# Optimization experiments

Measured on AMD Instinct MI355X. Metric: run time of the kernel, lower is better.

The kernel has to match this reference:

```python
import jax, jax.numpy as jnp
import numpy as np

N_NODES = 50000
N_FEAT = 128
HIDDEN = 3
N_EDGES = 600000
N_POWERS = 3


def setup_inputs() -> dict:
    key = jax.random.key(0)
    ks = jax.random.split(key, 6)
    x = jax.random.normal(ks[0], (N_NODES, N_FEAT), dtype=jnp.float32)
    edge_index = jax.random.randint(ks[1], (N_POWERS, 2, N_EDGES), 0, N_NODES, dtype=jnp.int64)
    # MLP params for the 3 adjacency powers, stacked on the leading axis.
    # torch Linear(in,out) stored transposed here: y = x @ W + b.
    Wa = jax.random.normal(ks[2], (N_POWERS, N_FEAT, HIDDEN), dtype=jnp.float32) * (1.0 / np.sqrt(N_FEAT))
    ba = jax.random.normal(ks[3], (N_POWERS, HIDDEN), dtype=jnp.float32) * 0.01
    Wb = jax.random.normal(ks[4], (N_POWERS, HIDDEN, 1), dtype=jnp.float32) * (1.0 / np.sqrt(HIDDEN))
    bb = jax.random.normal(ks[5], (N_POWERS, 1), dtype=jnp.float32) * 0.01
    return {"x": x, "edge_index": edge_index, "Wa": Wa, "ba": ba, "Wb": Wb, "bb": bb}


def reference(x, edge_index, Wa, ba, Wb, bb):
    # Gather source/target node features per edge, per adjacency power.
    x_j = x[edge_index[:, 0]]          # [P, E, F]
    x_i = x[edge_index[:, 1]]          # [P, E, F]
    abs_dif = jnp.abs(x_j - x_i)       # [P, E, F]
    # Tiny per-edge MLP: Linear -> ReLU -> Linear -> Sigmoid (separate params per power).
    h = jax.nn.relu(jnp.einsum('pef,pfh->peh', abs_dif, Wa) + ba[:, None, :])  # [P, E, H]
    w = jax.nn.sigmoid(jnp.einsum('peh,pho->peo', h, Wb) + bb[:, None, :])     # [P, E, 1]
    return w[..., 0]                   # [P, E] edge weights for each power
```

## Files before the change

### kernel.cpp

```cpp
#include <hip/hip_runtime.h>
#include <math.h>

#define N_NODES 50000
#define N_FEAT  128
#define N_EDGES 600000
#define N_POWERS 3

#define PAIRS 5
#define EDGES_PER_BLK (64 * PAIRS)

#define CAP 81920
#define NBUCK 8
#define CHUNK 2048
#define NCHUNK 293

typedef _Float16 half2v __attribute__((ext_vector_type(2)));
union HU { unsigned u; half2v h; };

__device__ __forceinline__ int bucket_of(int j) { return (int)(((unsigned)j * 41u) >> 18); }

__global__ __launch_bounds__(256) void conv_x_plain(const float* __restrict__ x,
                                                    unsigned* __restrict__ xh,
                                                    const float* __restrict__ Wa,
                                                    unsigned* __restrict__ wah) {
    const int t = blockIdx.x * 256 + threadIdx.x;
    const float4* x4 = (const float4*)x;
    float4 a = x4[(size_t)t * 2];
    float4 b = x4[(size_t)t * 2 + 1];
    HU p0, p1, p2, p3;
    p0.h = half2v{(_Float16)a.x, (_Float16)a.y};
    p1.h = half2v{(_Float16)a.z, (_Float16)a.w};
    p2.h = half2v{(_Float16)b.x, (_Float16)b.y};
    p3.h = half2v{(_Float16)b.z, (_Float16)b.w};
    ((uint4*)xh)[t] = uint4{p0.u, p1.u, p2.u, p3.u};
    if (blockIdx.x == 0 && threadIdx.x < 192) {
        const int tt = threadIdx.x;
        #pragma unroll
        for (int q = 0; q < 3; ++q) {
            int idx = tt + q * 192;
            int c  = idx % 3;
            int pk = idx / 3;
            int k  = pk % 64;
            int p  = pk / 64;
            float w0 = Wa[p * 384 + (2 * k) * 3 + c];
            float w1 = Wa[p * 384 + (2 * k + 1) * 3 + c];
            HU u; u.h = half2v{(_Float16)w0, (_Float16)w1};
            wah[idx] = u.u;
        }
    }
}

__global__ __launch_bounds__(256) void hist_kernel(const int* __restrict__ edge_index,
                                                   int* __restrict__ hist) {
    __shared__ int lh[NBUCK];
    const int p = blockIdx.y, chunk = blockIdx.x;
    if (threadIdx.x < NBUCK) lh[threadIdx.x] = 0;
    __syncthreads();
    const int* ej = edge_index + (size_t)p * 2 * N_EDGES;
    const int base = chunk * CHUNK;
    #pragma unroll
    for (int k = 0; k < 8; ++k) {
        const int e = base + k * 256 + threadIdx.x;
        if (e < N_EDGES) {
            const int j = __builtin_nontemporal_load(ej + e);
            atomicAdd(&lh[bucket_of(j)], 1);
        }
    }
    __syncthreads();
    if (threadIdx.x < NBUCK)
        hist[(p * NBUCK + threadIdx.x) * NCHUNK + chunk] = lh[threadIdx.x];
}

__global__ __launch_bounds__(64) void scan_hist(int* __restrict__ hist,
                                                int* __restrict__ cur) {
    const int pb = blockIdx.x;
    const int lane = threadIdx.x;
    int* h = hist + pb * NCHUNK;
    int carry = 0;
    for (int t = 0; t < NCHUNK; t += 64) {
        const int c = t + lane;
        int v = (c < NCHUNK) ? h[c] : 0;
        int s = v;
        #pragma unroll
        for (int d = 1; d < 64; d <<= 1) {
            int u = __shfl_up(s, d, 64);
            if (lane >= d) s += u;
        }
        if (c < NCHUNK) h[c] = carry + (s - v);
        carry += __shfl(s, 63, 64);
    }
    if (lane == 0) cur[pb] = carry;
}

__global__ __launch_bounds__(256) void scatter_pass(const int* __restrict__ edge_index,
                                                    const int* __restrict__ hist,
                                                    unsigned long long* __restrict__ su) {
    __shared__ int lc[NBUCK];
    const int p = blockIdx.y, chunk = blockIdx.x;
    if (threadIdx.x < NBUCK) lc[threadIdx.x] = 0;
    __syncthreads();
    const int* ej = edge_index + (size_t)p * 2 * N_EDGES;
    const int* ei = ej + N_EDGES;
    const int base = chunk * CHUNK;
    #pragma unroll
    for (int k = 0; k < 8; ++k) {
        const int e = base + k * 256 + threadIdx.x;
        if (e < N_EDGES) {
            const int j = __builtin_nontemporal_load(ej + e);
            const int i = __builtin_nontemporal_load(ei + e);
            const int b = bucket_of(j);
            const int pos = atomicAdd(&lc[b], 1);
            const int off = hist[(p * NBUCK + b) * NCHUNK + chunk];
            const size_t slot = (size_t)(p * NBUCK + b) * CAP + off + pos;
            su[slot] = (unsigned long long)(unsigned)(j | (i << 16))
                     | ((unsigned long long)e << 32);
        }
    }
}

template<int PAT>
__device__ __forceinline__ float swz(float v) {
    return __int_as_float(__builtin_amdgcn_ds_swizzle(__float_as_int(v), PAT));
}

__device__ __forceinline__ void dot3_8(const uint4& qa0, const uint4& qa1,
                                       const uint4& qb0, const uint4& qb1,
                                       const HU wa[8][3],
                                       float& h0, float& h1, float& h2) {
    unsigned ua[8] = {qa0.x, qa0.y, qa0.z, qa0.w, qa1.x, qa1.y, qa1.z, qa1.w};
    unsigned ub[8] = {qb0.x, qb0.y, qb0.z, qb0.w, qb1.x, qb1.y, qb1.z, qb1.w};
    h0 = 0.f; h1 = 0.f; h2 = 0.f;
    #pragma unroll
    for (int k = 0; k < 8; ++k) {
        HU a, b, d;
        a.u = ua[k]; b.u = ub[k];
        d.h = a.h - b.h;
        d.u &= 0x7fff7fffu;
        h0 = __builtin_amdgcn_fdot2(d.h, wa[k][0].h, h0, false);
        h1 = __builtin_amdgcn_fdot2(d.h, wa[k][1].h, h1, false);
        h2 = __builtin_amdgcn_fdot2(d.h, wa[k][2].h, h2, false);
    }
}

__global__ __launch_bounds__(256) void adj_kernel_sorted(
    const unsigned* __restrict__ xh,
    const unsigned long long* __restrict__ su,
    const int* __restrict__ cur,
    const unsigned* __restrict__ wah,
    const float* __restrict__ ba,
    const float* __restrict__ Wb,
    const float* __restrict__ bb,
    float* __restrict__ out)
{
    const int p    = blockIdx.y;
    const int b    = blockIdx.x & 7;
    const int k    = blockIdx.x >> 3;
    const int tid  = threadIdx.x;
    const int lane = tid & 63;
    const int wave = tid >> 6;
    const int sub  = lane & 7;
    const int grp  = lane >> 3;

    const int count = cur[p * NBUCK + b];
    const int base  = k * EDGES_PER_BLK;
    if (base >= count) return;

    HU wa[8][3];
    {
        const unsigned* wp = wah + ((size_t)p * 64 + sub * 8) * 3;
        #pragma unroll
        for (int kk = 0; kk < 8; ++kk) {
            wa[kk][0].u = wp[kk * 3 + 0];
            wa[kk][1].u = wp[kk * 3 + 1];
            wa[kk][2].u = wp[kk * 3 + 2];
        }
        #pragma unroll
        for (int kk = 0; kk < 8; ++kk) {
            asm volatile("" : "+v"(wa[kk][0].u), "+v"(wa[kk][1].u), "+v"(wa[kk][2].u));
        }
    }

    const float ba0 = ba[p * 3 + 0], ba1 = ba[p * 3 + 1], ba2 = ba[p * 3 + 2];
    const float wb0 = Wb[p * 3 + 0], wb1 = Wb[p * 3 + 1], wb2 = Wb[p * 3 + 2];
    const float bbp = bb[p];

    const unsigned long long* sup = su + (size_t)(p * NBUCK + b) * CAP;
    float* outp = out + (size_t)p * N_EDGES;

    const int eoff = wave * 8 + grp;
    const int roff = sub * 8;
    const int cm1  = count - 1;

    #pragma unroll
    for (int it = 0; it < PAIRS; ++it) {
        const int r1 = base + it * 64 + eoff;
        const int r2 = r1 + 32;
        const bool v1 = r1 < count;
        const bool v2 = r2 < count;
        const int s1 = min(r1, cm1);
        const int s2 = min(r2, cm1);

        const unsigned long long q1 = __builtin_nontemporal_load(sup + s1);
        const unsigned long long q2 = __builtin_nontemporal_load(sup + s2);
        const int j1 = (int)(q1 & 0xFFFFu);
        const int i1 = (int)((q1 >> 16) & 0xFFFFu);
        const int e1 = (int)(q1 >> 32);
        const int j2 = (int)(q2 & 0xFFFFu);
        const int i2 = (int)((q2 >> 16) & 0xFFFFu);
        const int e2 = (int)(q2 >> 32);

        const uint4* rj1 = (const uint4*)(xh + ((size_t)j1 << 6) + roff);
        const uint4* ri1 = (const uint4*)(xh + ((size_t)i1 << 6) + roff);
        const uint4* rj2 = (const uint4*)(xh + ((size_t)j2 << 6) + roff);
        const uint4* ri2 = (const uint4*)(xh + ((size_t)i2 << 6) + roff);
        uint4 a0 = rj1[0], a1 = rj1[1];
        uint4 b0 = ri1[0], b1 = ri1[1];
        uint4 c0 = rj2[0], c1 = rj2[1];
        uint4 d0 = ri2[0], d1 = ri2[1];

        float h0a, h1a, h2a, h0b, h1b, h2b;
        dot3_8(a0, a1, b0, b1, wa, h0a, h1a, h2a);
        dot3_8(c0, c1, d0, d1, wa, h0b, h1b, h2b);

        h0a += swz<0x041F>(h0a); h1a += swz<0x041F>(h1a); h2a += swz<0x041F>(h2a);
        h0b += swz<0x041F>(h0b); h1b += swz<0x041F>(h1b); h2b += swz<0x041F>(h2b);
        h0a += swz<0x081F>(h0a); h1a += swz<0x081F>(h1a); h2a += swz<0x081F>(h2a);
        h0b += swz<0x081F>(h0b); h1b += swz<0x081F>(h1b); h2b += swz<0x081F>(h2b);
        h0a += swz<0x101F>(h0a); h1a += swz<0x101F>(h1a); h2a += swz<0x101F>(h2a);
        h0b += swz<0x101F>(h0b); h1b += swz<0x101F>(h1b); h2b += swz<0x101F>(h2b);

        if (sub == 0) {
            if (v1) {
                float r0 = fmaxf(h0a + ba0, 0.f);
                float r1f = fmaxf(h1a + ba1, 0.f);
                float r2f = fmaxf(h2a + ba2, 0.f);
                float s  = fmaf(r0, wb0, fmaf(r1f, wb1, fmaf(r2f, wb2, bbp)));
                __builtin_nontemporal_store(1.f / (1.f + __expf(-s)), outp + e1);
            }
            if (v2) {
                float r0 = fmaxf(h0b + ba0, 0.f);
                float r1f = fmaxf(h1b + ba1, 0.f);
                float r2f = fmaxf(h2b + ba2, 0.f);
                float s  = fmaf(r0, wb0, fmaf(r1f, wb1, fmaf(r2f, wb2, bbp)));
                __builtin_nontemporal_store(1.f / (1.f + __expf(-s)), outp + e2);
            }
        }
    }
}

__global__ __launch_bounds__(256) void adj_kernel_f16(
    const unsigned* __restrict__ xh,
    const unsigned* __restrict__ wah,
    const int*   __restrict__ edge_index,
    const float* __restrict__ ba,
    const float* __restrict__ Wb,
    const float* __restrict__ bb,
    float* __restrict__ out)
{
    const int p    = blockIdx.y;
    const int tid  = threadIdx.x;
    const int lane = tid & 63;
    const int wave = tid >> 6;
    const int sub  = lane & 7;
    const int grp  = lane >> 3;

    HU wa[8][3];
    {
        const unsigned* wp = wah + ((size_t)p * 64 + sub * 8) * 3;
        #pragma unroll
        for (int k = 0; k < 8; ++k) {
            wa[k][0].u = wp[k * 3 + 0];
            wa[k][1].u = wp[k * 3 + 1];
            wa[k][2].u = wp[k * 3 + 2];
        }
        #pragma unroll
        for (int k = 0; k < 8; ++k) {
            asm volatile("" : "+v"(wa[k][0].u), "+v"(wa[k][1].u), "+v"(wa[k][2].u));
        }
    }

    const float ba0 = ba[p * 3 + 0], ba1 = ba[p * 3 + 1], ba2 = ba[p * 3 + 2];
    const float wb0 = Wb[p * 3 + 0], wb1 = Wb[p * 3 + 1], wb2 = Wb[p * 3 + 2];
    const float bbp = bb[p];

    const int* ej = edge_index + (size_t)p * 2 * N_EDGES;
    const int* ei = ej + N_EDGES;
    float* outp = out + (size_t)p * N_EDGES;

    const int e_blk = blockIdx.x * EDGES_PER_BLK;
    const int eoff  = wave * 8 + grp;
    const int roff  = sub * 8;

    #pragma unroll
    for (int it = 0; it < PAIRS; ++it) {
        const int e1 = e_blk + it * 64 + eoff;
        const int e2 = e1 + 32;
        const int j1 = __builtin_nontemporal_load(ej + e1);
        const int i1 = __builtin_nontemporal_load(ei + e1);
        const int j2 = __builtin_nontemporal_load(ej + e2);
        const int i2 = __builtin_nontemporal_load(ei + e2);

        const uint4* rj1 = (const uint4*)(xh + ((size_t)j1 << 6) + roff);
        const uint4* ri1 = (const uint4*)(xh + ((size_t)i1 << 6) + roff);
        const uint4* rj2 = (const uint4*)(xh + ((size_t)j2 << 6) + roff);
        const uint4* ri2 = (const uint4*)(xh + ((size_t)i2 << 6) + roff);
        uint4 a0 = rj1[0], a1 = rj1[1];
        uint4 b0 = ri1[0], b1 = ri1[1];
        uint4 c0 = rj2[0], c1 = rj2[1];
        uint4 d0 = ri2[0], d1 = ri2[1];

        float h0a, h1a, h2a, h0b, h1b, h2b;
        dot3_8(a0, a1, b0, b1, wa, h0a, h1a, h2a);
        dot3_8(c0, c1, d0, d1, wa, h0b, h1b, h2b);

        h0a += swz<0x041F>(h0a); h1a += swz<0x041F>(h1a); h2a += swz<0x041F>(h2a);
        h0b += swz<0x041F>(h0b); h1b += swz<0x041F>(h1b); h2b += swz<0x041F>(h2b);
        h0a += swz<0x081F>(h0a); h1a += swz<0x081F>(h1a); h2a += swz<0x081F>(h2a);
        h0b += swz<0x081F>(h0b); h1b += swz<0x081F>(h1b); h2b += swz<0x081F>(h2b);
        h0a += swz<0x101F>(h0a); h1a += swz<0x101F>(h1a); h2a += swz<0x101F>(h2a);
        h0b += swz<0x101F>(h0b); h1b += swz<0x101F>(h1b); h2b += swz<0x101F>(h2b);

        if (sub == 0) {
            float r0 = fmaxf(h0a + ba0, 0.f);
            float r1 = fmaxf(h1a + ba1, 0.f);
            float r2 = fmaxf(h2a + ba2, 0.f);
            float s  = fmaf(r0, wb0, fmaf(r1, wb1, fmaf(r2, wb2, bbp)));
            __builtin_nontemporal_store(1.f / (1.f + __expf(-s)), outp + e1);
            r0 = fmaxf(h0b + ba0, 0.f);
            r1 = fmaxf(h1b + ba1, 0.f);
            r2 = fmaxf(h2b + ba2, 0.f);
            s  = fmaf(r0, wb0, fmaf(r1, wb1, fmaf(r2, wb2, bbp)));
            __builtin_nontemporal_store(1.f / (1.f + __expf(-s)), outp + e2);
        }
    }
}

__global__ __launch_bounds__(256) void adj_kernel_f32(
    const float* __restrict__ x,
    const int*   __restrict__ edge_index,
    const float* __restrict__ Wa,
    const float* __restrict__ ba,
    const float* __restrict__ Wb,
    const float* __restrict__ bb,
    float* __restrict__ out)
{
    const int p    = blockIdx.y;
    const int tid  = threadIdx.x;
    const int lane = tid & 63;
    const int wave = tid >> 6;
    const int sub  = lane & 15;
    const int grp  = lane >> 4;
    const int f0 = sub * 8;

    const float* Wap = Wa + (size_t)p * N_FEAT * 3;
    float wa0[8], wa1[8], wa2[8];
    #pragma unroll
    for (int k = 0; k < 8; ++k) {
        wa0[k] = Wap[(f0 + k) * 3 + 0];
        wa1[k] = Wap[(f0 + k) * 3 + 1];
        wa2[k] = Wap[(f0 + k) * 3 + 2];
    }
    const float ba0 = ba[p * 3 + 0], ba1 = ba[p * 3 + 1], ba2 = ba[p * 3 + 2];
    const float wb0 = Wb[p * 3 + 0], wb1 = Wb[p * 3 + 1], wb2 = Wb[p * 3 + 2];
    const float bbp = bb[p];

    const int e = blockIdx.x * 16 + wave * 4 + grp;
    const int* ej = edge_index + (size_t)p * 2 * N_EDGES;
    const int* ei = ej + N_EDGES;
    const int j = ej[e];
    const int i = ei[e];

    const float4* xj = (const float4*)(x + (size_t)j * N_FEAT + f0);
    const float4* xi = (const float4*)(x + (size_t)i * N_FEAT + f0);
    float4 a0 = xj[0], a1 = xj[1];
    float4 b0 = xi[0], b1 = xi[1];

    float d[8];
    d[0] = fabsf(a0.x - b0.x); d[1] = fabsf(a0.y - b0.y);
    d[2] = fabsf(a0.z - b0.z); d[3] = fabsf(a0.w - b0.w);
    d[4] = fabsf(a1.x - b1.x); d[5] = fabsf(a1.y - b1.y);
    d[6] = fabsf(a1.z - b1.z); d[7] = fabsf(a1.w - b1.w);

    float h0 = 0.f, h1 = 0.f, h2 = 0.f;
    #pragma unroll
    for (int k = 0; k < 8; ++k) {
        h0 = fmaf(d[k], wa0[k], h0);
        h1 = fmaf(d[k], wa1[k], h1);
        h2 = fmaf(d[k], wa2[k], h2);
    }
    #pragma unroll
    for (int m = 1; m < 16; m <<= 1) {
        h0 += __shfl_xor(h0, m, 64);
        h1 += __shfl_xor(h1, m, 64);
        h2 += __shfl_xor(h2, m, 64);
    }
    if (sub == 0) {
        float r0 = fmaxf(h0 + ba0, 0.f);
        float r1 = fmaxf(h1 + ba1, 0.f);
        float r2 = fmaxf(h2 + ba2, 0.f);
        float s  = fmaf(r0, wb0, fmaf(r1, wb1, fmaf(r2, wb2, bbp)));
        float w  = 1.f / (1.f + expf(-s));
        out[(size_t)p * N_EDGES + e] = w;
    }
}

extern "C" void kernel_launch(void* const* d_in, const int* in_sizes, int n_in,
                              void* d_out, int out_size, void* d_ws, size_t ws_size,
                              hipStream_t stream) {
    const float* x          = (const float*)d_in[0];
    const int*   edge_index = (const int*)d_in[1];
    const float* Wa         = (const float*)d_in[2];
    const float* ba         = (const float*)d_in[3];
    const float* Wb         = (const float*)d_in[4];
    const float* bb         = (const float*)d_in[5];
    float* out = (float*)d_out;

    const size_t x_bytes    = (size_t)N_NODES * N_FEAT * 2;
    const size_t su_bytes   = (size_t)N_POWERS * NBUCK * CAP * 8;
    const size_t wa_bytes   = 2304;
    const size_t hist_bytes = (size_t)N_POWERS * NBUCK * NCHUNK * 4;
    const size_t cur_bytes  = NBUCK * N_POWERS * 4;
    const size_t need_full  = x_bytes + su_bytes + wa_bytes + hist_bytes + cur_bytes;

    if (ws_size >= need_full) {
        char* w = (char*)d_ws;
        unsigned* xh = (unsigned*)w;
        unsigned long long* su = (unsigned long long*)(w + x_bytes);
        unsigned* wah = (unsigned*)(w + x_bytes + su_bytes);
        int* hist = (int*)(w + x_bytes + su_bytes + wa_bytes);
        int* cur  = (int*)(w + x_bytes + su_bytes + wa_bytes + hist_bytes);

        conv_x_plain<<<N_NODES * N_FEAT / 2048, 256, 0, stream>>>(x, xh, Wa, wah);
        hist_kernel<<<dim3(NCHUNK, N_POWERS), 256, 0, stream>>>(edge_index, hist);
        scan_hist<<<NBUCK * N_POWERS, 64, 0, stream>>>(hist, cur);
        scatter_pass<<<dim3(NCHUNK, N_POWERS), 256, 0, stream>>>(edge_index, hist, su);
        dim3 grid(NBUCK * (CAP / EDGES_PER_BLK), N_POWERS);
        adj_kernel_sorted<<<grid, 256, 0, stream>>>(xh, su, cur, wah, ba, Wb, bb, out);
    } else if (ws_size >= x_bytes + wa_bytes) {
        unsigned* xh  = (unsigned*)d_ws;
        unsigned* wah = (unsigned*)((char*)d_ws + x_bytes);
        conv_x_plain<<<N_NODES * N_FEAT / 2048, 256, 0, stream>>>(x, xh, Wa, wah);
        dim3 grid(N_EDGES / EDGES_PER_BLK, N_POWERS);
        adj_kernel_f16<<<grid, 256, 0, stream>>>(xh, wah, edge_index, ba, Wb, bb, out);
    } else {
        dim3 grid((N_EDGES + 15) / 16, N_POWERS);
        adj_kernel_f32<<<grid, 256, 0, stream>>>(x, edge_index, Wa, ba, Wb, bb, out);
    }
}
```

Measured before the change: 177.1 us.

## Fuse conversion and histogram kernels; prefetch sorted edge records with 4 edges per group

The fp16 conversion of x and the bucket histogram are merged into a single prep kernel, which removes one launch and lets both run concurrently. The sorted adjacency kernel now processes 4 consecutive edges per 8-lane group over 4 iterations of 512 edges per block. It software-prefetches the next iteration's packed edge records while issuing the current row gathers, with a sched_barrier to hold that order. The scatter adds a capacity guard and uses nontemporal stores. In exchange, register pressure rises from holding 8 uint4 row pairs per thread plus prefetched records.

```diff
diff --git a/kernel.cpp b/kernel.cpp
--- a/kernel.cpp
+++ b/kernel.cpp
@@ -6,18 +6,245 @@
 #define N_EDGES 600000
 #define N_POWERS 3
 
-#define PAIRS 5
-#define EDGES_PER_BLK (64 * PAIRS)
-
+#define NBUCK 8
 #define CAP 81920
-#define NBUCK 8
 #define CHUNK 2048
 #define NCHUNK 293
+#define CONV_BLKS 3125
+
+#define ITERS 4
+#define EDGES_PER_BLK 512
 
 typedef _Float16 half2v __attribute__((ext_vector_type(2)));
 union HU { unsigned u; half2v h; };
 
-__device__ __forceinline__ int bucket_of(int j) { return (int)(((unsigned)j * 41u) >> 18); }
+__device__ __forceinline__ int slice_of(int v) { return (int)(((unsigned)v * 41u) >> 18); }
+
+__global__ __launch_bounds__(256) void prep_kernel(const float* __restrict__ x,
+                                                   unsigned* __restrict__ xh,
+                                                   const float* __restrict__ Wa,
+                                                   unsigned* __restrict__ wah,
+                                                   const int* __restrict__ edge_index,
+                                                   int* __restrict__ hist) {
+    const int bx = blockIdx.x;
+    if (bx < CONV_BLKS) {
+        const int t = bx * 256 + threadIdx.x;
+        const float4* x4 = (const float4*)x;
+        float4 a = x4[(size_t)t * 2];
+        float4 b = x4[(size_t)t * 2 + 1];
+        HU p0, p1, p2, p3;
+        p0.h = half2v{(_Float16)a.x, (_Float16)a.y};
+        p1.h = half2v{(_Float16)a.z, (_Float16)a.w};
+        p2.h = half2v{(_Float16)b.x, (_Float16)b.y};
+        p3.h = half2v{(_Float16)b.z, (_Float16)b.w};
+        ((uint4*)xh)[t] = uint4{p0.u, p1.u, p2.u, p3.u};
+        if (bx == 0 && threadIdx.x < 192) {
+            const int tt = threadIdx.x;
+            #pragma unroll
+            for (int q = 0; q < 3; ++q) {
+                int idx = tt + q * 192;
+                int c  = idx % 3;
+                int pk = idx / 3;
+                int k  = pk % 64;
+                int p  = pk / 64;
+                float w0 = Wa[p * 384 + (2 * k) * 3 + c];
+                float w1 = Wa[p * 384 + (2 * k + 1) * 3 + c];
+                HU u; u.h = half2v{(_Float16)w0, (_Float16)w1};
+                wah[idx] = u.u;
+            }
+        }
+    } else {
+        __shared__ int lh[NBUCK];
+        const int idx = bx - CONV_BLKS;
+        const int p = idx / NCHUNK;
+        const int chunk = idx - p * NCHUNK;
+        if (threadIdx.x < NBUCK) lh[threadIdx.x] = 0;
+        __syncthreads();
+        const int* ej = edge_index + (size_t)p * 2 * N_EDGES;
+        const int base = chunk * CHUNK;
+        #pragma unroll
+        for (int k = 0; k < 8; ++k) {
+            const int e = base + k * 256 + threadIdx.x;
+            if (e < N_EDGES) {
+                const int j = __builtin_nontemporal_load(ej + e);
+                atomicAdd(&lh[slice_of(j)], 1);
+            }
+        }
+        __syncthreads();
+        if (threadIdx.x < NBUCK)
+            hist[(p * NBUCK + threadIdx.x) * NCHUNK + chunk] = lh[threadIdx.x];
+    }
+}
+
+__global__ __launch_bounds__(64) void scan_hist(int* __restrict__ hist,
+                                                int* __restrict__ cur) {
+    const int pb = blockIdx.x;
+    const int lane = threadIdx.x;
+    int* h = hist + pb * NCHUNK;
+    int carry = 0;
+    for (int t = 0; t < NCHUNK; t += 64) {
+        const int c = t + lane;
+        int v = (c < NCHUNK) ? h[c] : 0;
+        int s = v;
+        #pragma unroll
+        for (int d = 1; d < 64; d <<= 1) {
+            int u = __shfl_up(s, d, 64);
+            if (lane >= d) s += u;
+        }
+        if (c < NCHUNK) h[c] = carry + (s - v);
+        carry += __shfl(s, 63, 64);
+    }
+    if (lane == 0) cur[pb] = carry;
+}
+
+__global__ __launch_bounds__(256) void scatter_pass(const int* __restrict__ edge_index,
+                                                    const int* __restrict__ hist,
+                                                    unsigned long long* __restrict__ su) {
+    __shared__ int lc[NBUCK];
+    const int p = blockIdx.y, chunk = blockIdx.x;
+    if (threadIdx.x < NBUCK) lc[threadIdx.x] = 0;
+    __syncthreads();
+    const int* ej = edge_index + (size_t)p * 2 * N_EDGES;
+    const int* ei = ej + N_EDGES;
+    const int base = chunk * CHUNK;
+    #pragma unroll
+    for (int k = 0; k < 8; ++k) {
+        const int e = base + k * 256 + threadIdx.x;
+        if (e < N_EDGES) {
+            const int j = __builtin_nontemporal_load(ej + e);
+            const int i = __builtin_nontemporal_load(ei + e);
+            const int b = slice_of(j);
+            const int pos = atomicAdd(&lc[b], 1);
+            const int off = hist[(p * NBUCK + b) * NCHUNK + chunk] + pos;
+            if (off < CAP) {
+                const size_t slot = (size_t)(p * NBUCK + b) * CAP + off;
+                __builtin_nontemporal_store(
+                    (unsigned long long)(((unsigned)i << 16) | (unsigned)j)
+                    | ((unsigned long long)(unsigned)e << 32), su + slot);
+            }
+        }
+    }
+}
+
+template<int PAT>
+__device__ __forceinline__ float swz(float v) {
+    return __int_as_float(__builtin_amdgcn_ds_swizzle(__float_as_int(v), PAT));
+}
+
+__device__ __forceinline__ void dot3_8(const uint4& qa0, const uint4& qa1,
+                                       const uint4& qb0, const uint4& qb1,
+                                       const HU wa[8][3],
+                                       float& h0, float& h1, float& h2) {
+    unsigned ua[8] = {qa0.x, qa0.y, qa0.z, qa0.w, qa1.x, qa1.y, qa1.z, qa1.w};
+    unsigned ub[8] = {qb0.x, qb0.y, qb0.z, qb0.w, qb1.x, qb1.y, qb1.z, qb1.w};
+    h0 = 0.f; h1 = 0.f; h2 = 0.f;
+    #pragma unroll
+    for (int k = 0; k < 8; ++k) {
+        HU a, b, d;
+        a.u = ua[k]; b.u = ub[k];
+        d.h = a.h - b.h;
+        d.u &= 0x7fff7fffu;
+        h0 = __builtin_amdgcn_fdot2(d.h, wa[k][0].h, h0, false);
+        h1 = __builtin_amdgcn_fdot2(d.h, wa[k][1].h, h1, false);
+        h2 = __builtin_amdgcn_fdot2(d.h, wa[k][2].h, h2, false);
+    }
+}
+
+__global__ __launch_bounds__(256) void adj_kernel_f16x4(
+    const unsigned* __restrict__ xh,
+    const unsigned long long* __restrict__ su,
+    const int* __restrict__ cur,
+    const unsigned* __restrict__ wah,
+    const float* __restrict__ ba,
+    const float* __restrict__ Wb,
+    const float* __restrict__ bb,
+    float* __restrict__ out)
+{
+    const int p    = blockIdx.y;
+    const int jb   = blockIdx.x & 7;
+    const int kblk = blockIdx.x >> 3;
+    const int tid  = threadIdx.x;
+    const int lane = tid & 63;
+    const int wave = tid >> 6;
+    const int sub  = lane & 7;
+    const int grp  = lane >> 3;
+
+    const int bidx  = p * NBUCK + jb;
+    const int count = min(cur[bidx], CAP);
+    const int base  = kblk * EDGES_PER_BLK;
+    if (base >= count) return;
+
+    HU wa[8][3];
+    {
+        const unsigned* wp = wah + ((size_t)p * 64 + sub * 8) * 3;
+        #pragma unroll
+        for (int k = 0; k < 8; ++k) {
+            wa[k][0].u = wp[k * 3 + 0];
+            wa[k][1].u = wp[k * 3 + 1];
+            wa[k][2].u = wp[k * 3 + 2];
+        }
+        #pragma unroll
+        for (int k = 0; k < 8; ++k)
+            asm volatile("" : "+v"(wa[k][0].u), "+v"(wa[k][1].u), "+v"(wa[k][2].u));
+    }
+
+    const float ba0 = ba[p * 3 + 0], ba1 = ba[p * 3 + 1], ba2 = ba[p * 3 + 2];
+    const float wb0 = Wb[p * 3 + 0], wb1 = Wb[p * 3 + 1], wb2 = Wb[p * 3 + 2];
+    const float bbp = bb[p];
+
+    const unsigned long long* sup = su + (size_t)bidx * CAP;
+    float* outp = out + (size_t)p * N_EDGES;
+    const int roff = sub * 8;
+    const int cm1  = count - 1;
+    const int goff = wave * 32 + grp * 4;
+
+    unsigned long long q0 = sup[min(base + goff + 0, cm1)];
+    unsigned long long q1 = sup[min(base + goff + 1, cm1)];
+    unsigned long long q2 = sup[min(base + goff + 2, cm1)];
+    unsigned long long q3 = sup[min(base + goff + 3, cm1)];
+
+    #pragma unroll
+    for (int it = 0; it < ITERS; ++it) {
+        const int rr = base + it * 128 + goff;
+        const unsigned long long qq[4] = {q0, q1, q2, q3};
+
+        uint4 RJ[4][2], RI[4][2];
+        #pragma unroll
+        for (int e = 0; e < 4; ++e) {
+            const int j = (int)(qq[e] & 0xFFFFu);
+            const int i = (int)((qq[e] >> 16) & 0xFFFFu);
+            const uint4* rj = (const uint4*)(xh + ((size_t)j << 6) + roff);
+            const uint4* ri = (const uint4*)(xh + ((size_t)i << 6) + roff);
+            RJ[e][0] = rj[0]; RJ[e][1] = rj[1];
+            RI[e][0] = ri[0]; RI[e][1] = ri[1];
+        }
+        if (it + 1 < ITERS) {
+            const int rn = rr + 128;
+            q0 = sup[min(rn + 0, cm1)];
+            q1 = sup[min(rn + 1, cm1)];
+            q2 = sup[min(rn + 2, cm1)];
+            q3 = sup[min(rn + 3, cm1)];
+        }
+        __builtin_amdgcn_sched_barrier(0);
+
+        #pragma unroll
+        for (int e = 0; e < 4; ++e) {
+            float h0, h1, h2;
+            dot3_8(RJ[e][0], RJ[e][1], RI[e][0], RI[e][1], wa, h0, h1, h2);
+            h0 += swz<0x041F>(h0); h1 += swz<0x041F>(h1); h2 += swz<0x041F>(h2);
+            h0 += swz<0x081F>(h0); h1 += swz<0x081F>(h1); h2 += swz<0x081F>(h2);
+            h0 += swz<0x101F>(h0); h1 += swz<0x101F>(h1); h2 += swz<0x101F>(h2);
+            if (sub == 0 && (rr + e) < count) {
+                const int eo = (int)(qq[e] >> 32);
+                float r0 = fmaxf(h0 + ba0, 0.f);
+                float r1 = fmaxf(h1 + ba1, 0.f);
+                float r2 = fmaxf(h2 + ba2, 0.f);
+                float s  = fmaf(r0, wb0, fmaf(r1, wb1, fmaf(r2, wb2, bbp)));
+                __builtin_nontemporal_store(1.f / (1.f + __expf(-s)), outp + eo);
+            }
+        }
+    }
+}
 
 __global__ __launch_bounds__(256) void conv_x_plain(const float* __restrict__ x,
                                                     unsigned* __restrict__ xh,
@@ -50,204 +277,6 @@
     }
 }
 
-__global__ __launch_bounds__(256) void hist_kernel(const int* __restrict__ edge_index,
-                                                   int* __restrict__ hist) {
-    __shared__ int lh[NBUCK];
-    const int p = blockIdx.y, chunk = blockIdx.x;
-    if (threadIdx.x < NBUCK) lh[threadIdx.x] = 0;
-    __syncthreads();
-    const int* ej = edge_index + (size_t)p * 2 * N_EDGES;
-    const int base = chunk * CHUNK;
-    #pragma unroll
-    for (int k = 0; k < 8; ++k) {
-        const int e = base + k * 256 + threadIdx.x;
-        if (e < N_EDGES) {
-            const int j = __builtin_nontemporal_load(ej + e);
-            atomicAdd(&lh[bucket_of(j)], 1);
-        }
-    }
-    __syncthreads();
-    if (threadIdx.x < NBUCK)
-        hist[(p * NBUCK + threadIdx.x) * NCHUNK + chunk] = lh[threadIdx.x];
-}
-
-__global__ __launch_bounds__(64) void scan_hist(int* __restrict__ hist,
-                                                int* __restrict__ cur) {
-    const int pb = blockIdx.x;
-    const int lane = threadIdx.x;
-    int* h = hist + pb * NCHUNK;
-    int carry = 0;
-    for (int t = 0; t < NCHUNK; t += 64) {
-        const int c = t + lane;
-        int v = (c < NCHUNK) ? h[c] : 0;
-        int s = v;
-        #pragma unroll
-        for (int d = 1; d < 64; d <<= 1) {
-            int u = __shfl_up(s, d, 64);
-            if (lane >= d) s += u;
-        }
-        if (c < NCHUNK) h[c] = carry + (s - v);
-        carry += __shfl(s, 63, 64);
-    }
-    if (lane == 0) cur[pb] = carry;
-}
-
-__global__ __launch_bounds__(256) void scatter_pass(const int* __restrict__ edge_index,
-                                                    const int* __restrict__ hist,
-                                                    unsigned long long* __restrict__ su) {
-    __shared__ int lc[NBUCK];
-    const int p = blockIdx.y, chunk = blockIdx.x;
-    if (threadIdx.x < NBUCK) lc[threadIdx.x] = 0;
-    __syncthreads();
-    const int* ej = edge_index + (size_t)p * 2 * N_EDGES;
-    const int* ei = ej + N_EDGES;
-    const int base = chunk * CHUNK;
-    #pragma unroll
-    for (int k = 0; k < 8; ++k) {
-        const int e = base + k * 256 + threadIdx.x;
-        if (e < N_EDGES) {
-            const int j = __builtin_nontemporal_load(ej + e);
-            const int i = __builtin_nontemporal_load(ei + e);
-            const int b = bucket_of(j);
-            const int pos = atomicAdd(&lc[b], 1);
-            const int off = hist[(p * NBUCK + b) * NCHUNK + chunk];
-            const size_t slot = (size_t)(p * NBUCK + b) * CAP + off + pos;
-            su[slot] = (unsigned long long)(unsigned)(j | (i << 16))
-                     | ((unsigned long long)e << 32);
-        }
-    }
-}
-
-template<int PAT>
-__device__ __forceinline__ float swz(float v) {
-    return __int_as_float(__builtin_amdgcn_ds_swizzle(__float_as_int(v), PAT));
-}
-
-__device__ __forceinline__ void dot3_8(const uint4& qa0, const uint4& qa1,
-                                       const uint4& qb0, const uint4& qb1,
-                                       const HU wa[8][3],
-                                       float& h0, float& h1, float& h2) {
-    unsigned ua[8] = {qa0.x, qa0.y, qa0.z, qa0.w, qa1.x, qa1.y, qa1.z, qa1.w};
-    unsigned ub[8] = {qb0.x, qb0.y, qb0.z, qb0.w, qb1.x, qb1.y, qb1.z, qb1.w};
-    h0 = 0.f; h1 = 0.f; h2 = 0.f;
-    #pragma unroll
-    for (int k = 0; k < 8; ++k) {
-        HU a, b, d;
-        a.u = ua[k]; b.u = ub[k];
-        d.h = a.h - b.h;
-        d.u &= 0x7fff7fffu;
-        h0 = __builtin_amdgcn_fdot2(d.h, wa[k][0].h, h0, false);
-        h1 = __builtin_amdgcn_fdot2(d.h, wa[k][1].h, h1, false);
-        h2 = __builtin_amdgcn_fdot2(d.h, wa[k][2].h, h2, false);
-    }
-}
-
-__global__ __launch_bounds__(256) void adj_kernel_sorted(
-    const unsigned* __restrict__ xh,
-    const unsigned long long* __restrict__ su,
-    const int* __restrict__ cur,
-    const unsigned* __restrict__ wah,
-    const float* __restrict__ ba,
-    const float* __restrict__ Wb,
-    const float* __restrict__ bb,
-    float* __restrict__ out)
-{
-    const int p    = blockIdx.y;
-    const int b    = blockIdx.x & 7;
-    const int k    = blockIdx.x >> 3;
-    const int tid  = threadIdx.x;
-    const int lane = tid & 63;
-    const int wave = tid >> 6;
-    const int sub  = lane & 7;
-    const int grp  = lane >> 3;
-
-    const int count = cur[p * NBUCK + b];
-    const int base  = k * EDGES_PER_BLK;
-    if (base >= count) return;
-
-    HU wa[8][3];
-    {
-        const unsigned* wp = wah + ((size_t)p * 64 + sub * 8) * 3;
-        #pragma unroll
-        for (int kk = 0; kk < 8; ++kk) {
-            wa[kk][0].u = wp[kk * 3 + 0];
-            wa[kk][1].u = wp[kk * 3 + 1];
-            wa[kk][2].u = wp[kk * 3 + 2];
-        }
-        #pragma unroll
-        for (int kk = 0; kk < 8; ++kk) {
-            asm volatile("" : "+v"(wa[kk][0].u), "+v"(wa[kk][1].u), "+v"(wa[kk][2].u));
-        }
-    }
-
-    const float ba0 = ba[p * 3 + 0], ba1 = ba[p * 3 + 1], ba2 = ba[p * 3 + 2];
-    const float wb0 = Wb[p * 3 + 0], wb1 = Wb[p * 3 + 1], wb2 = Wb[p * 3 + 2];
-    const float bbp = bb[p];
-
-    const unsigned long long* sup = su + (size_t)(p * NBUCK + b) * CAP;
-    float* outp = out + (size_t)p * N_EDGES;
-
-    const int eoff = wave * 8 + grp;
-    const int roff = sub * 8;
-    const int cm1  = count - 1;
-
-    #pragma unroll
-    for (int it = 0; it < PAIRS; ++it) {
-        const int r1 = base + it * 64 + eoff;
-        const int r2 = r1 + 32;
-        const bool v1 = r1 < count;
-        const bool v2 = r2 < count;
-        const int s1 = min(r1, cm1);
-        const int s2 = min(r2, cm1);
-
-        const unsigned long long q1 = __builtin_nontemporal_load(sup + s1);
-        const unsigned long long q2 = __builtin_nontemporal_load(sup + s2);
-        const int j1 = (int)(q1 & 0xFFFFu);
-        const int i1 = (int)((q1 >> 16) & 0xFFFFu);
-        const int e1 = (int)(q1 >> 32);
-        const int j2 = (int)(q2 & 0xFFFFu);
-        const int i2 = (int)((q2 >> 16) & 0xFFFFu);
-        const int e2 = (int)(q2 >> 32);
-
-        const uint4* rj1 = (const uint4*)(xh + ((size_t)j1 << 6) + roff);
-        const uint4* ri1 = (const uint4*)(xh + ((size_t)i1 << 6) + roff);
-        const uint4* rj2 = (const uint4*)(xh + ((size_t)j2 << 6) + roff);
-        const uint4* ri2 = (const uint4*)(xh + ((size_t)i2 << 6) + roff);
-        uint4 a0 = rj1[0], a1 = rj1[1];
-        uint4 b0 = ri1[0], b1 = ri1[1];
-        uint4 c0 = rj2[0], c1 = rj2[1];
-        uint4 d0 = ri2[0], d1 = ri2[1];
-
-        float h0a, h1a, h2a, h0b, h1b, h2b;
-        dot3_8(a0, a1, b0, b1, wa, h0a, h1a, h2a);
-        dot3_8(c0, c1, d0, d1, wa, h0b, h1b, h2b);
-
-        h0a += swz<0x041F>(h0a); h1a += swz<0x041F>(h1a); h2a += swz<0x041F>(h2a);
-        h0b += swz<0x041F>(h0b); h1b += swz<0x041F>(h1b); h2b += swz<0x041F>(h2b);
-        h0a += swz<0x081F>(h0a); h1a += swz<0x081F>(h1a); h2a += swz<0x081F>(h2a);
-        h0b += swz<0x081F>(h0b); h1b += swz<0x081F>(h1b); h2b += swz<0x081F>(h2b);
-        h0a += swz<0x101F>(h0a); h1a += swz<0x101F>(h1a); h2a += swz<0x101F>(h2a);
-        h0b += swz<0x101F>(h0b); h1b += swz<0x101F>(h1b); h2b += swz<0x101F>(h2b);
-
-        if (sub == 0) {
-            if (v1) {
-                float r0 = fmaxf(h0a + ba0, 0.f);
-                float r1f = fmaxf(h1a + ba1, 0.f);
-                float r2f = fmaxf(h2a + ba2, 0.f);
-                float s  = fmaf(r0, wb0, fmaf(r1f, wb1, fmaf(r2f, wb2, bbp)));
-                __builtin_nontemporal_store(1.f / (1.f + __expf(-s)), outp + e1);
-            }
-            if (v2) {
-                float r0 = fmaxf(h0b + ba0, 0.f);
-                float r1f = fmaxf(h1b + ba1, 0.f);
-                float r2f = fmaxf(h2b + ba2, 0.f);
-                float s  = fmaf(r0, wb0, fmaf(r1f, wb1, fmaf(r2f, wb2, bbp)));
-                __builtin_nontemporal_store(1.f / (1.f + __expf(-s)), outp + e2);
-            }
-        }
-    }
-}
-
 __global__ __launch_bounds__(256) void adj_kernel_f16(
     const unsigned* __restrict__ xh,
     const unsigned* __restrict__ wah,
@@ -274,9 +303,8 @@
             wa[k][2].u = wp[k * 3 + 2];
         }
         #pragma unroll
-        for (int k = 0; k < 8; ++k) {
+        for (int k = 0; k < 8; ++k)
             asm volatile("" : "+v"(wa[k][0].u), "+v"(wa[k][1].u), "+v"(wa[k][2].u));
-        }
     }
 
     const float ba0 = ba[p * 3 + 0], ba1 = ba[p * 3 + 1], ba2 = ba[p * 3 + 2];
@@ -287,12 +315,12 @@
     const int* ei = ej + N_EDGES;
     float* outp = out + (size_t)p * N_EDGES;
 
-    const int e_blk = blockIdx.x * EDGES_PER_BLK;
+    const int e_blk = blockIdx.x * 320;
     const int eoff  = wave * 8 + grp;
     const int roff  = sub * 8;
 
     #pragma unroll
-    for (int it = 0; it < PAIRS; ++it) {
+    for (int it = 0; it < 5; ++it) {
         const int e1 = e_blk + it * 64 + eoff;
         const int e2 = e1 + 32;
         const int j1 = __builtin_nontemporal_load(ej + e1);
@@ -417,30 +445,30 @@
 
     const size_t x_bytes    = (size_t)N_NODES * N_FEAT * 2;
     const size_t su_bytes   = (size_t)N_POWERS * NBUCK * CAP * 8;
-    const size_t wa_bytes   = 2304;
+    const size_t wah_bytes  = 2304;
     const size_t hist_bytes = (size_t)N_POWERS * NBUCK * NCHUNK * 4;
     const size_t cur_bytes  = NBUCK * N_POWERS * 4;
-    const size_t need_full  = x_bytes + su_bytes + wa_bytes + hist_bytes + cur_bytes;
+    const size_t need_full  = x_bytes + su_bytes + wah_bytes + hist_bytes + cur_bytes;
 
     if (ws_size >= need_full) {
         char* w = (char*)d_ws;
         unsigned* xh = (unsigned*)w;
         unsigned long long* su = (unsigned long long*)(w + x_bytes);
         unsigned* wah = (unsigned*)(w + x_bytes + su_bytes);
-        int* hist = (int*)(w + x_bytes + su_bytes + wa_bytes);
-        int* cur  = (int*)(w + x_bytes + su_bytes + wa_bytes + hist_bytes);
-
-        conv_x_plain<<<N_NODES * N_FEAT / 2048, 256, 0, stream>>>(x, xh, Wa, wah);
-        hist_kernel<<<dim3(NCHUNK, N_POWERS), 256, 0, stream>>>(edge_index, hist);
+        int* hist = (int*)(w + x_bytes + su_bytes + wah_bytes);
+        int* cur  = (int*)(w + x_bytes + su_bytes + wah_bytes + hist_bytes);
+
+        prep_kernel<<<CONV_BLKS + NCHUNK * N_POWERS, 256, 0, stream>>>(x, xh, Wa, wah,
+                                                                       edge_index, hist);
         scan_hist<<<NBUCK * N_POWERS, 64, 0, stream>>>(hist, cur);
         scatter_pass<<<dim3(NCHUNK, N_POWERS), 256, 0, stream>>>(edge_index, hist, su);
         dim3 grid(NBUCK * (CAP / EDGES_PER_BLK), N_POWERS);
-        adj_kernel_sorted<<<grid, 256, 0, stream>>>(xh, su, cur, wah, ba, Wb, bb, out);
-    } else if (ws_size >= x_bytes + wa_bytes) {
+        adj_kernel_f16x4<<<grid, 256, 0, stream>>>(xh, su, cur, wah, ba, Wb, bb, out);
+    } else if (ws_size >= x_bytes + wah_bytes) {
         unsigned* xh  = (unsigned*)d_ws;
         unsigned* wah = (unsigned*)((char*)d_ws + x_bytes);
         conv_x_plain<<<N_NODES * N_FEAT / 2048, 256, 0, stream>>>(x, xh, Wa, wah);
-        dim3 grid(N_EDGES / EDGES_PER_BLK, N_POWERS);
+        dim3 grid(N_EDGES / 320, N_POWERS);
         adj_kernel_f16<<<grid, 256, 0, stream>>>(xh, wah, edge_index, ba, Wb, bb, out);
     } else {
         dim3 grid((N_EDGES + 15) / 16, N_POWERS);
```

Result: slower. 200.1 us (+13.0%).
